# Performance work log

Measured on AMD Instinct MI355X. Metric: run time of the kernel, lower is better.

The kernel has to match this reference:

```python
import jax, jax.numpy as jnp
import numpy as np

GAMMA = 2.5
K = 4
RHO = 0.085
TAU_CLIP = 5.0
NUM_HEADS = 8


def setup_inputs() -> dict:
    key = jax.random.key(0)
    ks = jax.random.split(key, 4)
    B, T, C = 2, 2048, 512
    x = jax.random.normal(ks[0], (B, T, C), jnp.float32)
    tau = jax.random.uniform(ks[1], (B, T, T), jnp.float32)
    s = 1.0 / np.sqrt(C)
    Wqkv = jax.random.normal(ks[2], (C, 3 * C), jnp.float32) * s
    bqkv = jnp.zeros((3 * C,), jnp.float32)
    Wproj = jax.random.normal(ks[3], (C, C), jnp.float32) * s
    bproj = jnp.zeros((C,), jnp.float32)
    return dict(x=x, tau=tau, Wqkv=Wqkv, bqkv=bqkv, Wproj=Wproj, bproj=bproj)


def reference(x, tau, Wqkv, bqkv, Wproj, bproj):
    B, T, C = x.shape
    H = NUM_HEADS
    D = C // H
    qkv = x @ Wqkv + bqkv                       # [B,T,3C]
    q, k, v = jnp.split(qkv, 3, axis=-1)
    q = q.reshape(B, T, H, D).transpose(0, 2, 1, 3)   # [B,H,T,D]
    k = k.reshape(B, T, H, D).transpose(0, 2, 1, 3)
    v = v.reshape(B, T, H, D).transpose(0, 2, 1, 3)
    scale = D ** -0.5
    logits = jnp.einsum('bhtd,bhsd->bhts', q, k) * scale   # [B,H,T,T]
    pheromone_bias = GAMMA * jnp.log(tau + 1e-8)           # [B,T,T]
    logits = logits + pheromone_bias[:, None]
    # top-K keys per query from tau define the sparse mask (LOCAL_WINDOW=0)
    k_val = min(K, T)
    idx = jax.lax.top_k(tau, k_val)[1]                     # [B,T,K]
    mask = jnp.zeros((B, T, T), bool).at[
        jnp.arange(B)[:, None, None], jnp.arange(T)[None, :, None], idx
    ].set(True)
    logits = jnp.where(mask[:, None], logits, -jnp.inf)
    attn = jax.nn.softmax(logits, axis=-1)                 # [B,H,T,T]
    # EMA pheromone (tau) update, no gradient in original (torch.no_grad)
    signal = attn.mean(axis=1)                             # [B,T,T]
    tau_new = (1.0 - RHO) * tau + signal ** 3
    tau_new = tau_new / (tau_new.sum(axis=-1, keepdims=True) + 1e-8)
    tau_new = jnp.minimum(tau_new, TAU_CLIP)
    tau_new = jax.lax.stop_gradient(tau_new)
    out = jnp.einsum('bhts,bhsd->bthd', attn, v).reshape(B, T, C)
    out = out @ Wproj + bproj
    return out, tau_new
```

## Files before the change

### kernel.cpp

```cpp
#include <hip/hip_runtime.h>
#include <hip/hip_bf16.h>
#include <math.h>

#define BB 2
#define TT 2048
#define CC 512
#define HH 8
#define DD 64
#define KK 4
#define C3 1536
#define MROWS (BB*TT)

#define G1_NT (C3/64)
#define G1_BLOCKS (G1_NT*(MROWS/128))
#define G2_NT (CC/64)
#define G2_BLOCKS (G2_NT*(MROWS/128))

typedef __attribute__((ext_vector_type(8))) short bf16x8;
typedef __attribute__((ext_vector_type(4))) float floatx4;

static __device__ __forceinline__ unsigned short f2bf(float f) {
  unsigned int u = __float_as_uint(f);
  return (unsigned short)((u + 0x7fffu + ((u >> 16) & 1u)) >> 16);
}
static __device__ __forceinline__ float bf2f(unsigned short u) {
  return __uint_as_float(((unsigned int)u) << 16);
}

template<bool BF16OUT>
static __device__ __forceinline__ void gemm_body(
    int bid, int nt,
    const unsigned short* __restrict__ A,
    const unsigned short* __restrict__ Bt,
    const float* __restrict__ bias,
    void* __restrict__ Cout, int N, int K) {
  __shared__ bf16x8 As[128 * 4];
  __shared__ bf16x8 Bs[64 * 4];
  const int tid  = threadIdx.x;
  const int wave = tid >> 6;
  const int lane = tid & 63;
  const int n0 = (bid % nt) * 64;
  const int m0 = (bid / nt) * 128;
  const int m_off = (wave >> 1) * 64;
  const int n_off = (wave & 1) * 32;
  const int lrow = lane >> 2;
  const int lcol = (lane & 3) * 8;
  const int fr = lane & 15;
  const int fq = lane >> 4;

  floatx4 acc[4][2];
#pragma unroll
  for (int i = 0; i < 4; ++i)
#pragma unroll
    for (int j = 0; j < 2; ++j) acc[i][j] = (floatx4){0.f, 0.f, 0.f, 0.f};

  for (int k0 = 0; k0 < K; k0 += 32) {
#pragma unroll
    for (int s = 0; s < 2; ++s) {
      int q = wave * 2 + s;
      const unsigned short* ga = A + (size_t)(m0 + q * 16 + lrow) * K + k0 + lcol;
      __builtin_amdgcn_global_load_lds(
          (const __attribute__((address_space(1))) void*)ga,
          (__attribute__((address_space(3))) void*)((char*)As + q * 1024), 16, 0, 0);
    }
    const unsigned short* gb = Bt + (size_t)(n0 + wave * 16 + lrow) * K + k0 + lcol;
    __builtin_amdgcn_global_load_lds(
        (const __attribute__((address_space(1))) void*)gb,
        (__attribute__((address_space(3))) void*)((char*)Bs + wave * 1024), 16, 0, 0);
    __syncthreads();
    bf16x8 a[4], b[2];
#pragma unroll
    for (int i = 0; i < 4; ++i) a[i] = As[(m_off + i * 16 + fr) * 4 + fq];
#pragma unroll
    for (int j = 0; j < 2; ++j) b[j] = Bs[(n_off + j * 16 + fr) * 4 + fq];
#pragma unroll
    for (int i = 0; i < 4; ++i)
#pragma unroll
      for (int j = 0; j < 2; ++j)
        acc[i][j] = __builtin_amdgcn_mfma_f32_16x16x32_bf16(a[i], b[j], acc[i][j], 0, 0, 0);
    __syncthreads();
  }
#pragma unroll
  for (int j = 0; j < 2; ++j) {
    int col = n0 + n_off + j * 16 + fr;
    float bv = bias[col];
#pragma unroll
    for (int i = 0; i < 4; ++i) {
#pragma unroll
      for (int r = 0; r < 4; ++r) {
        int row = m0 + m_off + i * 16 + fq * 4 + r;
        float v = acc[i][j][r] + bv;
        if (BF16OUT) ((unsigned short*)Cout)[(size_t)row * N + col] = f2bf(v);
        else         ((float*)Cout)[(size_t)row * N + col] = v;
      }
    }
  }
}

static __device__ __forceinline__ void topk_body(
    int row, const float* __restrict__ tau, int* __restrict__ idx_out) {
  const int tid = threadIdx.x;
  const float4* rp = (const float4*)(tau + (size_t)row * TT);
  float v[8];
  float4 f0 = rp[tid * 2], f1 = rp[tid * 2 + 1];
  v[0]=f0.x; v[1]=f0.y; v[2]=f0.z; v[3]=f0.w;
  v[4]=f1.x; v[5]=f1.y; v[6]=f1.z; v[7]=f1.w;
  __shared__ float wv[4];
  __shared__ int wi[4];
  __shared__ int winner;
  const int base = tid * 8;
  int chosen[KK];
  for (int r = 0; r < KK; ++r) {
    float bv = v[0]; int bi = base;
#pragma unroll
    for (int i = 1; i < 8; ++i)
      if (v[i] > bv) { bv = v[i]; bi = base + i; }
#pragma unroll
    for (int off = 32; off > 0; off >>= 1) {
      float vv = __shfl_xor(bv, off, 64);
      int   ii = __shfl_xor(bi, off, 64);
      if (vv > bv || (vv == bv && ii < bi)) { bv = vv; bi = ii; }
    }
    if ((tid & 63) == 0) { wv[tid >> 6] = bv; wi[tid >> 6] = bi; }
    __syncthreads();
    if (tid == 0) {
      float b2 = wv[0]; int i2 = wi[0];
      for (int k = 1; k < 4; ++k)
        if (wv[k] > b2 || (wv[k] == b2 && wi[k] < i2)) { b2 = wv[k]; i2 = wi[k]; }
      winner = i2;
    }
    __syncthreads();
    int win = winner;
    chosen[r] = win;
    if ((win >> 3) == tid) v[win & 7] = -1e30f;
    __syncthreads();
  }
  if (tid < KK) idx_out[row * KK + tid] = chosen[tid];
}

static __device__ __forceinline__ void tau_body(
    int row, const float* __restrict__ tau, const int* __restrict__ idx_in,
    const float* __restrict__ sig_in, float* __restrict__ tau_out) {
  const int tid = threadIdx.x;
  int i4[KK]; float s3[KK];
#pragma unroll
  for (int j = 0; j < KK; ++j) {
    i4[j] = idx_in[row * KK + j];
    float s = sig_in[row * KK + j];
    s3[j] = s * s * s;
  }
  const float4* rp = (const float4*)(tau + (size_t)row * TT);
  float v[8];
  float4 f0 = rp[tid * 2], f1 = rp[tid * 2 + 1];
  v[0]=f0.x; v[1]=f0.y; v[2]=f0.z; v[3]=f0.w;
  v[4]=f1.x; v[5]=f1.y; v[6]=f1.z; v[7]=f1.w;
  const float keep = 1.0f - 0.085f;
  const int base = tid * 8;
  float local = 0.f;
#pragma unroll
  for (int i = 0; i < 8; ++i) {
    float t = keep * v[i];
#pragma unroll
    for (int j = 0; j < KK; ++j)
      if (base + i == i4[j]) t += s3[j];
    v[i] = t;
    local += t;
  }
#pragma unroll
  for (int off = 32; off > 0; off >>= 1) local += __shfl_xor(local, off, 64);
  __shared__ float wsum[4];
  __shared__ float tot;
  if ((tid & 63) == 0) wsum[tid >> 6] = local;
  __syncthreads();
  if (tid == 0) tot = wsum[0] + wsum[1] + wsum[2] + wsum[3];
  __syncthreads();
  float inv = 1.f / (tot + 1e-8f);
  float4* op = (float4*)(tau_out + (size_t)row * TT);
  float4 o0 = { fminf(v[0]*inv,5.f), fminf(v[1]*inv,5.f), fminf(v[2]*inv,5.f), fminf(v[3]*inv,5.f) };
  float4 o1 = { fminf(v[4]*inv,5.f), fminf(v[5]*inv,5.f), fminf(v[6]*inv,5.f), fminf(v[7]*inv,5.f) };
  op[tid * 2] = o0;
  op[tid * 2 + 1] = o1;
}

static __device__ __forceinline__ void transpose_body(
    int t, int nbx, const float* __restrict__ W, unsigned short* __restrict__ Wt,
    int R, int Cn) {
  __shared__ unsigned short tile[32][33];
  const int c0 = (t % nbx) * 32, r0 = (t / nbx) * 32;
  const int tx = threadIdx.x & 31, ty = threadIdx.x >> 5;
#pragma unroll
  for (int i = 0; i < 4; ++i) {
    int r = ty + i * 8;
    tile[r][tx] = f2bf(W[(size_t)(r0 + r) * Cn + c0 + tx]);
  }
  __syncthreads();
#pragma unroll
  for (int i = 0; i < 4; ++i) {
    int r = ty + i * 8;
    Wt[(size_t)(c0 + r) * R + r0 + tx] = tile[tx][r];
  }
}

__global__ __launch_bounds__(256) void prep_kernel(
    const float* __restrict__ x, unsigned short* __restrict__ x_bf,
    const float* __restrict__ Wqkv, unsigned short* __restrict__ wqkv_t,
    const float* __restrict__ Wproj, unsigned short* __restrict__ wproj_t) {
  const int bid = blockIdx.x;
  if (bid < 1024) {
    int g = bid * 256 + threadIdx.x;
    const float4* p = (const float4*)x;
    float4 f0 = p[g * 2], f1 = p[g * 2 + 1];
    union { unsigned short u[8]; uint4 v; } pk;
    pk.u[0]=f2bf(f0.x); pk.u[1]=f2bf(f0.y); pk.u[2]=f2bf(f0.z); pk.u[3]=f2bf(f0.w);
    pk.u[4]=f2bf(f1.x); pk.u[5]=f2bf(f1.y); pk.u[6]=f2bf(f1.z); pk.u[7]=f2bf(f1.w);
    ((uint4*)x_bf)[g] = pk.v;
  } else if (bid < 1024 + 768) {
    transpose_body(bid - 1024, C3 / 32, Wqkv, wqkv_t, CC, C3);
  } else {
    transpose_body(bid - 1792, CC / 32, Wproj, wproj_t, CC, CC);
  }
}

__global__ __launch_bounds__(256) void gemm1_topk_kernel(
    const unsigned short* __restrict__ x_bf,
    const unsigned short* __restrict__ wqkv_t,
    const float* __restrict__ bqkv, unsigned short* __restrict__ qkv_bf,
    const float* __restrict__ tau, int* __restrict__ idx_out) {
  if (blockIdx.x < G1_BLOCKS)
    gemm_body<true>(blockIdx.x, G1_NT, x_bf, wqkv_t, bqkv, qkv_bf, C3, CC);
  else
    topk_body(blockIdx.x - G1_BLOCKS, tau, idx_out);
}

__global__ __launch_bounds__(512) void attn_kernel(
    const unsigned short* __restrict__ qkv, const float* __restrict__ tau,
    const int* __restrict__ idx_in, unsigned short* __restrict__ attn_bf,
    float* __restrict__ sig_out) {
  const int row  = blockIdx.x;
  const int b    = row >> 11;
  const int tid  = threadIdx.x;
  const int h    = tid >> 6;
  const int lane = tid & 63;

  __shared__ int   idx4[KK];
  __shared__ float tau4[KK];
  __shared__ float ps[HH][KK];
  if (tid < KK) {
    int s = idx_in[row * KK + tid];
    idx4[tid] = s;
    tau4[tid] = tau[(size_t)row * TT + s];
  }
  __syncthreads();

  const float q = bf2f(qkv[(size_t)row * C3 + h * DD + lane]);
  int   sidx[KK];
  float logit[KK];
#pragma unroll
  for (int j = 0; j < KK; ++j) {
    sidx[j] = idx4[j];
    float kv = bf2f(qkv[((size_t)(b * TT + sidx[j])) * C3 + CC + h * DD + lane]);
    float p = q * kv;
#pragma unroll
    for (int off = 32; off > 0; off >>= 1) p += __shfl_xor(p, off, 64);
    logit[j] = p * 0.125f + 2.5f * logf(tau4[j] + 1e-8f);
  }

  float m = fmaxf(fmaxf(logit[0], logit[1]), fmaxf(logit[2], logit[3]));
  float p[KK], den = 0.f;
#pragma unroll
  for (int j = 0; j < KK; ++j) { p[j] = expf(logit[j] - m); den += p[j]; }
  float inv = 1.f / den;
#pragma unroll
  for (int j = 0; j < KK; ++j) p[j] *= inv;

  float o = 0.f;
#pragma unroll
  for (int j = 0; j < KK; ++j)
    o += p[j] * bf2f(qkv[((size_t)(b * TT + sidx[j])) * C3 + 2 * CC + h * DD + lane]);
  attn_bf[(size_t)row * CC + h * DD + lane] = f2bf(o);

  if (lane < KK) ps[h][lane] = p[lane];
  __syncthreads();
  if (tid < KK) {
    float s = 0.f;
#pragma unroll
    for (int k = 0; k < HH; ++k) s += ps[k][tid];
    sig_out[row * KK + tid] = s * (1.0f / HH);
  }
}

__global__ __launch_bounds__(256) void gemm2_tau_kernel(
    const unsigned short* __restrict__ attn_bf,
    const unsigned short* __restrict__ wproj_t,
    const float* __restrict__ bproj, float* __restrict__ out,
    const float* __restrict__ tau, const int* __restrict__ idx_in,
    const float* __restrict__ sig_in, float* __restrict__ tau_out) {
  if (blockIdx.x < G2_BLOCKS)
    gemm_body<false>(blockIdx.x, G2_NT, attn_bf, wproj_t, bproj, out, CC, CC);
  else
    tau_body(blockIdx.x - G2_BLOCKS, tau, idx_in, sig_in, tau_out);
}

extern "C" void kernel_launch(void* const* d_in, const int* in_sizes, int n_in,
                              void* d_out, int out_size, void* d_ws, size_t ws_size,
                              hipStream_t stream) {
  const float* x     = (const float*)d_in[0];
  const float* tau   = (const float*)d_in[1];
  const float* Wqkv  = (const float*)d_in[2];
  const float* bqkv  = (const float*)d_in[3];
  const float* Wproj = (const float*)d_in[4];
  const float* bproj = (const float*)d_in[5];

  float* out     = (float*)d_out;
  float* tau_new = out + (size_t)MROWS * CC;

  char* w = (char*)d_ws;
  unsigned short* qkv_bf  = (unsigned short*)w; w += (size_t)MROWS * C3 * 2;
  unsigned short* x_bf    = (unsigned short*)w; w += (size_t)MROWS * CC * 2;
  unsigned short* wqkv_t  = (unsigned short*)w; w += (size_t)C3 * CC * 2;
  unsigned short* wproj_t = (unsigned short*)w; w += (size_t)CC * CC * 2;
  unsigned short* attn_bf = (unsigned short*)w; w += (size_t)MROWS * CC * 2;
  int*   idx = (int*)w;                  w += (size_t)MROWS * KK * 4;
  float* sig = (float*)w;

  prep_kernel<<<2048, 256, 0, stream>>>(x, x_bf, Wqkv, wqkv_t, Wproj, wproj_t);

  gemm1_topk_kernel<<<G1_BLOCKS + MROWS, 256, 0, stream>>>(
      x_bf, wqkv_t, bqkv, qkv_bf, tau, idx);

  attn_kernel<<<MROWS, 512, 0, stream>>>(qkv_bf, tau, idx, attn_bf, sig);

  gemm2_tau_kernel<<<G2_BLOCKS + MROWS, 256, 0, stream>>>(
      attn_bf, wproj_t, bproj, out, tau, idx, sig, tau_new);
}
```

Measured before the change: 150.6 us.

## Swizzle GEMM LDS tiles, use per-thread top-4 merge, batch attention gathers

```diff
diff --git a/kernel.cpp b/kernel.cpp
--- a/kernel.cpp
+++ b/kernel.cpp
@@ -44,9 +44,10 @@
   const int m_off = (wave >> 1) * 64;
   const int n_off = (wave & 1) * 32;
   const int lrow = lane >> 2;
-  const int lcol = (lane & 3) * 8;
+  const int lx   = ((lane & 3) ^ ((lane >> 3) & 3)) * 8;
   const int fr = lane & 15;
   const int fq = lane >> 4;
+  const int key = (fr >> 1) & 3;
 
   floatx4 acc[4][2];
 #pragma unroll
@@ -58,21 +59,23 @@
 #pragma unroll
     for (int s = 0; s < 2; ++s) {
       int q = wave * 2 + s;
-      const unsigned short* ga = A + (size_t)(m0 + q * 16 + lrow) * K + k0 + lcol;
+      const unsigned short* ga = A + (size_t)(m0 + q * 16 + lrow) * K + k0 + lx;
       __builtin_amdgcn_global_load_lds(
           (const __attribute__((address_space(1))) void*)ga,
           (__attribute__((address_space(3))) void*)((char*)As + q * 1024), 16, 0, 0);
     }
-    const unsigned short* gb = Bt + (size_t)(n0 + wave * 16 + lrow) * K + k0 + lcol;
+    const unsigned short* gb = Bt + (size_t)(n0 + wave * 16 + lrow) * K + k0 + lx;
     __builtin_amdgcn_global_load_lds(
         (const __attribute__((address_space(1))) void*)gb,
         (__attribute__((address_space(3))) void*)((char*)Bs + wave * 1024), 16, 0, 0);
     __syncthreads();
     bf16x8 a[4], b[2];
 #pragma unroll
-    for (int i = 0; i < 4; ++i) a[i] = As[(m_off + i * 16 + fr) * 4 + fq];
-#pragma unroll
-    for (int j = 0; j < 2; ++j) b[j] = Bs[(n_off + j * 16 + fr) * 4 + fq];
+    for (int i = 0; i < 4; ++i)
+      a[i] = As[(m_off + i * 16 + fr) * 4 + (fq ^ key)];
+#pragma unroll
+    for (int j = 0; j < 2; ++j)
+      b[j] = Bs[(n_off + j * 16 + fr) * 4 + (fq ^ key)];
 #pragma unroll
     for (int i = 0; i < 4; ++i)
 #pragma unroll
@@ -97,45 +100,87 @@
   }
 }
 
+static __device__ __forceinline__ bool kv_better(float av, int ai, float bv, int bi) {
+  return av > bv || (av == bv && ai < bi);
+}
+static __device__ __forceinline__ void kv_ce(float* v, int* i, int a, int b) {
+  if (!kv_better(v[a], i[a], v[b], i[b])) {
+    float tv = v[a]; v[a] = v[b]; v[b] = tv;
+    int   ti = i[a]; i[a] = i[b]; i[b] = ti;
+  }
+}
+static __device__ __forceinline__ void kv_merge(
+    float* av, int* ai, const float* bv, const int* bi) {
+  float cv[4]; int ci[4];
+#pragma unroll
+  for (int j = 0; j < 4; ++j) {
+    bool t = kv_better(av[j], ai[j], bv[3 - j], bi[3 - j]);
+    cv[j] = t ? av[j] : bv[3 - j];
+    ci[j] = t ? ai[j] : bi[3 - j];
+  }
+  kv_ce(cv, ci, 0, 2); kv_ce(cv, ci, 1, 3);
+  kv_ce(cv, ci, 0, 1); kv_ce(cv, ci, 2, 3);
+#pragma unroll
+  for (int j = 0; j < 4; ++j) { av[j] = cv[j]; ai[j] = ci[j]; }
+}
+
 static __device__ __forceinline__ void topk_body(
     int row, const float* __restrict__ tau, int* __restrict__ idx_out) {
   const int tid = threadIdx.x;
   const float4* rp = (const float4*)(tau + (size_t)row * TT);
-  float v[8];
   float4 f0 = rp[tid * 2], f1 = rp[tid * 2 + 1];
-  v[0]=f0.x; v[1]=f0.y; v[2]=f0.z; v[3]=f0.w;
-  v[4]=f1.x; v[5]=f1.y; v[6]=f1.z; v[7]=f1.w;
-  __shared__ float wv[4];
-  __shared__ int wi[4];
-  __shared__ int winner;
+  float e[8] = { f0.x, f0.y, f0.z, f0.w, f1.x, f1.y, f1.z, f1.w };
   const int base = tid * 8;
-  int chosen[KK];
-  for (int r = 0; r < KK; ++r) {
-    float bv = v[0]; int bi = base;
-#pragma unroll
-    for (int i = 1; i < 8; ++i)
-      if (v[i] > bv) { bv = v[i]; bi = base + i; }
-#pragma unroll
-    for (int off = 32; off > 0; off >>= 1) {
-      float vv = __shfl_xor(bv, off, 64);
-      int   ii = __shfl_xor(bi, off, 64);
-      if (vv > bv || (vv == bv && ii < bi)) { bv = vv; bi = ii; }
+
+  float tv[4] = { -1e30f, -1e30f, -1e30f, -1e30f };
+  int   ti[4] = { 1 << 30, 1 << 30, 1 << 30, 1 << 30 };
+#pragma unroll
+  for (int k = 0; k < 8; ++k) {
+    float v = e[k];
+    if (v > tv[3]) {
+      tv[3] = v; ti[3] = base + k;
+      if (tv[3] > tv[2]) { float a=tv[2]; tv[2]=tv[3]; tv[3]=a; int b=ti[2]; ti[2]=ti[3]; ti[3]=b; }
+      if (tv[2] > tv[1]) { float a=tv[1]; tv[1]=tv[2]; tv[2]=a; int b=ti[1]; ti[1]=ti[2]; ti[2]=b; }
+      if (tv[1] > tv[0]) { float a=tv[0]; tv[0]=tv[1]; tv[1]=a; int b=ti[0]; ti[0]=ti[1]; ti[1]=b; }
     }
-    if ((tid & 63) == 0) { wv[tid >> 6] = bv; wi[tid >> 6] = bi; }
-    __syncthreads();
-    if (tid == 0) {
-      float b2 = wv[0]; int i2 = wi[0];
-      for (int k = 1; k < 4; ++k)
-        if (wv[k] > b2 || (wv[k] == b2 && wi[k] < i2)) { b2 = wv[k]; i2 = wi[k]; }
-      winner = i2;
+  }
+
+#pragma unroll
+  for (int step = 1; step <= 32; step <<= 1) {
+    float bv[4]; int bi[4];
+#pragma unroll
+    for (int j = 0; j < 4; ++j) {
+      bv[j] = __shfl_xor(tv[j], step, 64);
+      bi[j] = __shfl_xor(ti[j], step, 64);
     }
-    __syncthreads();
-    int win = winner;
-    chosen[r] = win;
-    if ((win >> 3) == tid) v[win & 7] = -1e30f;
-    __syncthreads();
-  }
-  if (tid < KK) idx_out[row * KK + tid] = chosen[tid];
+    kv_merge(tv, ti, bv, bi);
+  }
+
+  __shared__ float swv[4][4];
+  __shared__ int   swi[4][4];
+  const int wave = tid >> 6, lane = tid & 63;
+  if (lane == 0) {
+#pragma unroll
+    for (int j = 0; j < 4; ++j) { swv[wave][j] = tv[j]; swi[wave][j] = ti[j]; }
+  }
+  __syncthreads();
+  if (tid == 0) {
+    float m0[4], m1[4]; int x0[4], x1[4];
+#pragma unroll
+    for (int j = 0; j < 4; ++j) { m0[j] = swv[0][j]; x0[j] = swi[0][j]; }
+#pragma unroll
+    for (int j = 0; j < 4; ++j) { m1[j] = swv[1][j]; x1[j] = swi[1][j]; }
+    kv_merge(m0, x0, m1, x1);
+#pragma unroll
+    for (int j = 0; j < 4; ++j) { m1[j] = swv[2][j]; x1[j] = swi[2][j]; }
+    float m2[4]; int x2[4];
+#pragma unroll
+    for (int j = 0; j < 4; ++j) { m2[j] = swv[3][j]; x2[j] = swi[3][j]; }
+    kv_merge(m1, x1, m2, x2);
+    kv_merge(m0, x0, m1, x1);
+    int4 w = { x0[0], x0[1], x0[2], x0[3] };
+    *((int4*)(idx_out + row * KK)) = w;
+  }
 }
 
 static __device__ __forceinline__ void tau_body(
@@ -253,20 +298,29 @@
   __syncthreads();
 
   const float q = bf2f(qkv[(size_t)row * C3 + h * DD + lane]);
-  int   sidx[KK];
+  float kv[KK], vv[KK];
+#pragma unroll
+  for (int j = 0; j < KK; ++j) {
+    size_t bs = ((size_t)(b * TT + idx4[j])) * C3 + h * DD + lane;
+    kv[j] = bf2f(qkv[bs + CC]);
+    vv[j] = bf2f(qkv[bs + 2 * CC]);
+  }
+
+  float p[KK];
+#pragma unroll
+  for (int j = 0; j < KK; ++j) p[j] = q * kv[j];
+#pragma unroll
+  for (int off = 32; off > 0; off >>= 1)
+#pragma unroll
+    for (int j = 0; j < KK; ++j) p[j] += __shfl_xor(p[j], off, 64);
+
   float logit[KK];
 #pragma unroll
-  for (int j = 0; j < KK; ++j) {
-    sidx[j] = idx4[j];
-    float kv = bf2f(qkv[((size_t)(b * TT + sidx[j])) * C3 + CC + h * DD + lane]);
-    float p = q * kv;
-#pragma unroll
-    for (int off = 32; off > 0; off >>= 1) p += __shfl_xor(p, off, 64);
-    logit[j] = p * 0.125f + 2.5f * logf(tau4[j] + 1e-8f);
-  }
+  for (int j = 0; j < KK; ++j)
+    logit[j] = p[j] * 0.125f + 2.5f * logf(tau4[j] + 1e-8f);
 
   float m = fmaxf(fmaxf(logit[0], logit[1]), fmaxf(logit[2], logit[3]));
-  float p[KK], den = 0.f;
+  float den = 0.f;
 #pragma unroll
   for (int j = 0; j < KK; ++j) { p[j] = expf(logit[j] - m); den += p[j]; }
   float inv = 1.f / den;
@@ -275,8 +329,7 @@
 
   float o = 0.f;
 #pragma unroll
-  for (int j = 0; j < KK; ++j)
-    o += p[j] * bf2f(qkv[((size_t)(b * TT + sidx[j])) * C3 + 2 * CC + h * DD + lane]);
+  for (int j = 0; j < KK; ++j) o += p[j] * vv[j];
   attn_bf[(size_t)row * CC + h * DD + lane] = f2bf(o);
 
   if (lane < KK) ps[h][lane] = p[lane];
```

After: 146.3 us. -2.9%, faster.
